# Performance work log

Measured on AMD Instinct MI355X. Metric: run time of the kernel, lower is better.

## Reference

```python
import jax, jax.numpy as jnp
import numpy as np

DN = ('NCHW', 'OIHW', 'NCHW')


def conv(x, W, s, p):
    return jax.lax.conv_general_dilated(x, W, (s, s), [(p, p), (p, p)], dimension_numbers=DN)


def conv_t(y, W, s, p, op):
    # F.conv_transpose2d(y, W, stride=s, padding=p, output_padding=op)
    k = W.shape[2]
    Wt = jnp.flip(W, (2, 3)).transpose(1, 0, 2, 3)  # (I,O,k,k) -> OIHW for the transpose conv
    pad = (k - 1 - p, k - 1 - p + op)
    return jax.lax.conv_general_dilated(y, Wt, (1, 1), [pad, pad], lhs_dilation=(s, s), dimension_numbers=DN)


def build_blk(weight_specs, ms, g, n):
    # blk_diag[r, c, g, m, n'] accumulation exactly as in the torch nested loops
    blk = jnp.zeros((ms, ms, g, n, n), dtype=weight_specs[0][0].dtype)
    for (W, stride, k) in weight_specs:
        A = W.reshape(W.shape[0], g, n, k, k)  # (O, g, n, k, k)
        ATA = jnp.einsum('ogmab,ognab->abgmn', A, A)  # (k, k, g, n, n)
        offset = ((stride - k) // 2) % stride  # k odd branch of the torch code
        for i1 in range(k):
            for j1 in range(k):
                for r in range((i1 + offset) % stride, ms, stride):
                    for c in range((j1 + offset) % stride, ms, stride):
                        blk = blk.at[r, c].add(ATA[i1, j1])
    return blk


def sub_diag(Z, X, blk, ms, g, n):
    b, c, h, w = X.shape
    X0 = X.reshape(b, g, n, h // ms, ms, w // ms, ms)
    Yd = jnp.einsum('rcgmn,bgnhrwc->bgmhrwc', blk, X0)
    return Z - Yd.reshape(b, c, h, w)


def hollow_forward(x0, x1, W00, W10, W11, b0, b1, g):
    # multiply: Y_i = sum_j conv(X_j)
    Y0 = conv(x0, W00, 1, 2)                       # (B,16,258,258)
    Y1 = conv(x0, W10, 2, 3) + conv(x1, W11, 1, 2)  # (B,32,130,130)
    # multiply_transpose: Z_j = sum_i conv_t(Y_i)
    Z0 = conv_t(Y0, W00, 1, 2, 0) + conv_t(Y1, W10, 2, 3, 1)  # (B,16,256,256)
    Z1 = conv_t(Y1, W11, 1, 2, 0)                             # (B,32,128,128)
    # block-diagonal self-term subtraction
    blk0 = build_blk([(W00, 1, 3), (W10, 2, 3)], ms=2, g=1, n=16)
    blk1 = build_blk([(W11, 1, 3)], ms=1, g=2, n=16)
    Z0 = sub_diag(Z0, x0, blk0, 2, 1, 16)
    Z1 = sub_diag(Z1, x1, blk1, 1, 2, 16)
    # bias term: y -= bias/||bias|| * g[i]; return -y
    Z0 = Z0 - (b0 / jnp.linalg.norm(b0)) * g[0]
    Z1 = Z1 - (b1 / jnp.linalg.norm(b1)) * g[1]
    return (-Z0, -Z1)


def setup_inputs() -> dict:
    key = jax.random.key(0)
    ks = jax.random.split(key, 8)
    B = 16
    x0 = jax.random.normal(ks[0], (B, 16, 256, 256), dtype=jnp.float32)
    x1 = jax.random.normal(ks[1], (B, 32, 128, 128), dtype=jnp.float32)
    # conv weights (PyTorch OIHW layout), modest scale ~ 1/sqrt(fan_in*k*k)
    W00 = jax.random.normal(ks[2], (16, 16, 3, 3), dtype=jnp.float32) * 0.08
    W10 = jax.random.normal(ks[3], (32, 16, 3, 3), dtype=jnp.float32) * 0.08
    W11 = jax.random.normal(ks[4], (32, 32, 3, 3), dtype=jnp.float32) * 0.06
    b0 = jax.random.uniform(ks[5], (16, 256, 256), dtype=jnp.float32)
    b1 = jax.random.uniform(ks[6], (32, 128, 128), dtype=jnp.float32)
    g = jnp.ones((2,), dtype=jnp.float32)
    return {'x0': x0, 'x1': x1, 'W00': W00, 'W10': W10, 'W11': W11, 'b0': b0, 'b1': b1, 'g': g}


def reference(x0, x1, W00, W10, W11, b0, b1, g):
    return hollow_forward(x0, x1, W00, W10, W11, b0, b1, g)
```

## Files before the change

### kernel.cpp

```cpp
#include <hip/hip_runtime.h>
#include <stdint.h>


using short8 = __attribute__((ext_vector_type(8))) short;
using f32x4  = __attribute__((ext_vector_type(4))) float;

#define B_ 16

static constexpr size_t Y1T_OFF  = 0;
static constexpr size_t Y1T_ROWB = 132 * 64;
static constexpr size_t X1T_OFF  = (size_t)16 * 130 * 132 * 64;
static constexpr size_t AB0_OFF  = X1T_OFF + (size_t)16 * 128 * 128 * 64;
static constexpr size_t AB1_OFF  = AB0_OFF + 24 * 1024;
static constexpr size_t SUM_OFF  = AB1_OFF + 20 * 1024;
static constexpr size_t AB2_OFF  = SUM_OFF + 1024;
static constexpr size_t PART_OFF = AB2_OFF + 56 * 1024;

__device__ __forceinline__ uint32_t bf16rne(float v) {
  uint32_t u = __float_as_uint(v);
  return (u + 0x7fffu + ((u >> 16) & 1u)) >> 16;
}
__device__ __forceinline__ uint32_t packbf(float lo, float hi) {
  return bf16rne(lo) | (bf16rne(hi) << 16);
}
__device__ __forceinline__ f32x4 mfma16(short8 a, short8 b, f32x4 c) {
  return __builtin_amdgcn_mfma_f32_16x16x32_bf16(a, b, c, 0, 0, 0);
}
__device__ __forceinline__ int xcd_swz(int bid, int chunk) {
  return (bid & 7) * chunk + (bid >> 3);
}

__global__ __launch_bounds__(256) void prep_k(const float* __restrict__ x1,
                                              const float* __restrict__ W00,
                                              const float* __restrict__ W10,
                                              const float* __restrict__ W11,
                                              const float* __restrict__ b0,
                                              const float* __restrict__ b1,
                                              char* __restrict__ ws) {
  __shared__ __align__(16) uint16_t tmp[128 * 32];
  int raw = blockIdx.x, tid = threadIdx.x;

  if (raw < 2048) {
    int b = raw >> 7, r = raw & 127;
    for (int e = tid; e < 4096; e += 256) {
      int ch = e >> 7, c = e & 127;
      float v = x1[((size_t)(b * 32 + ch) * 128 + r) * 128 + c];
      tmp[c * 32 + ch] = (uint16_t)bf16rne(v);
    }
    __syncthreads();
    char* dst = ws + X1T_OFF + ((size_t)(b * 128 + r) * 128) * 64;
    for (int e = tid; e < 512; e += 256)
      *(short8*)(dst + e * 16) = *(const short8*)((const char*)tmp + e * 16);
    return;
  }

  if (raw < 2248) {
    int e = (raw - 2048) * 256 + tid;
    if (e < 12288) {
      int chunk = e >> 9, le = e & 511, lane = le >> 3, j = le & 7;
      int q = lane >> 4, m = lane & 15;
      float val = 0.f;
      if (chunk < 13) {
        int t = 2 * chunk + (q >> 1);
        int n = ((q & 1) << 3) + j;
        if (t <= 24 && t != 12) {
          int dy = t / 5 - 2, dx = t % 5 - 2;
          for (int o = 0; o < 16; ++o) {
            const float* wm = W00 + (o * 16 + m) * 9;
            const float* wn = W00 + (o * 16 + n) * 9;
            for (int ay = 0; ay < 3; ++ay) {
              int ay2 = ay + dy; if ((unsigned)ay2 > 2u) continue;
              for (int ax = 0; ax < 3; ++ax) {
                int ax2 = ax + dx; if ((unsigned)ax2 > 2u) continue;
                val += wm[ay * 3 + ax] * wn[ay2 * 3 + ax2];
              }
            }
          }
        }
      } else if (chunk < 22) {
        int tap = chunk - 13;
        int o = ((lane >> 4) << 3) + j;
        val = W10[(o * 16 + m) * 9 + tap];
      } else {
        int py = chunk - 22;
        int k = ((lane >> 4) << 3) + j;
        int par = k >> 4, n = k & 15;
        for (int o = 0; o < 32; ++o) {
          const float* wn = W10 + (o * 16 + n) * 9;
          const float* wm = W10 + (o * 16 + m) * 9;
          for (int by = 0; by < 3; ++by) {
            if ((py == 0) ? (by != 1) : (by == 1)) continue;
            for (int bx = 0; bx < 3; ++bx) {
              if ((par == 0) ? (bx != 1) : (bx == 1)) continue;
              val -= wn[by * 3 + bx] * wm[by * 3 + bx];
            }
          }
        }
      }
      ((uint16_t*)(ws + AB0_OFF))[chunk * 512 + lane * 8 + j] = (uint16_t)bf16rne(val);
    } else if (e < 12288 + 10240) {
      int e2 = e - 12288;
      int chunk = e2 >> 10, r = e2 & 1023, h = r >> 9, le = r & 511;
      int lane = le >> 3, j = le & 7;
      int m = h * 16 + (lane & 15);
      int kk = ((lane >> 4) << 3) + j;
      float val = 0.f;
      if (chunk < 9) {
        val = W11[(kk * 32 + m) * 9 + chunk];
      } else if ((kk >> 4) == h) {
        int np = kk & 15;
        float s = 0.f;
        for (int o = 0; o < 32; ++o)
          for (int t = 0; t < 9; ++t)
            s += W11[(o * 32 + m) * 9 + t] * W11[(o * 32 + h * 16 + np) * 9 + t];
        val = -s;
      }
      ((uint16_t*)(ws + AB1_OFF))[(chunk * 2 + h) * 512 + lane * 8 + j] = (uint16_t)bf16rne(val);
    } else if (e < 12288 + 10240 + 28672) {
      int e3 = e - 22528;
      int chunk = e3 >> 9, le = e3 & 511;
      int lane = le >> 3, j = le & 7;
      int q = lane >> 4, m = lane & 15;
      int k = q * 8 + j;
      int part;
      float val = 0.f;
      if (chunk < 36) {
        int t = chunk >> 2, h = (chunk >> 1) & 1;
        part = chunk & 1;
        int o = h * 16 + m;
        val = W11[(o * 32 + k) * 9 + t];
      } else {
        int c2 = chunk - 36;
        int c5 = c2 >> 2, h = (c2 >> 1) & 1;
        part = c2 & 1;
        int tap = 2 * c5 + (k >> 4);
        int o = h * 16 + m;
        if (tap <= 8) val = W10[(o * 16 + (k & 15)) * 9 + tap];
      }
      uint32_t hi = bf16rne(val);
      uint16_t outv;
      if (part == 0) outv = (uint16_t)hi;
      else outv = (uint16_t)bf16rne(val - __uint_as_float(hi << 16));
      ((uint16_t*)(ws + AB2_OFF))[chunk * 512 + lane * 8 + j] = outv;
    }
    return;
  }

  float* part = (float*)(ws + PART_OFF);
  if (raw < 2312) {
    int blk = raw - 2248;
    float s = 0.f;
    for (int i = blk * 256 + tid; i < 1048576; i += 64 * 256) {
      float v = b0[i]; s += v * v;
    }
    #pragma unroll
    for (int off = 32; off > 0; off >>= 1) s += __shfl_down(s, off, 64);
    if ((tid & 63) == 0) part[blk * 4 + (tid >> 6)] = s;
  } else {
    int blk = raw - 2312;
    float s = 0.f;
    for (int i = blk * 256 + tid; i < 524288; i += 32 * 256) {
      float v = b1[i]; s += v * v;
    }
    #pragma unroll
    for (int off = 32; off > 0; off >>= 1) s += __shfl_down(s, off, 64);
    if ((tid & 63) == 0) part[256 + blk * 4 + (tid >> 6)] = s;
  }
}

__global__ __launch_bounds__(256, 5) void y1m_k(const float* __restrict__ x0,
                                                char* __restrict__ ws) {
  __shared__ __align__(16) uint16_t x0s[2 * 3 * 2 * 146 * 8];
  int tid = threadIdx.x;
  if (blockIdx.x >= 2080) {
    if (blockIdx.x == 2080) {
      int lane = tid & 63, wvv = tid >> 6;
      const float* part = (const float*)(ws + PART_OFF);
      if (wvv == 0) {
        float s = part[lane * 4] + part[lane * 4 + 1] + part[lane * 4 + 2] + part[lane * 4 + 3];
        #pragma unroll
        for (int off = 32; off > 0; off >>= 1) s += __shfl_down(s, off, 64);
        if (lane == 0) ((float*)(ws + SUM_OFF))[0] = s;
      } else if (wvv == 1) {
        float s = part[256 + lane * 2] + part[256 + lane * 2 + 1];
        #pragma unroll
        for (int off = 32; off > 0; off >>= 1) s += __shfl_down(s, off, 64);
        if (lane == 0) ((float*)(ws + SUM_OFF))[1] = s;
      }
    }
    return;
  }
  int bid = xcd_swz(blockIdx.x, 260);
  int b = bid / 130, iy = bid % 130;

  {
    uint4 z = make_uint4(0u, 0u, 0u, 0u);
    for (int e = tid; e < 1752; e += 256) ((uint4*)x0s)[e] = z;
  }
  __syncthreads();

  {
    const float* x0b = x0 + (size_t)b * 1048576;
    for (int e = tid; e < 6144; e += 256) {
      int r = e >> 11;
      int ch0 = ((e >> 8) & 7) * 2;
      int c = e & 255;
      int gy = 2 * iy + r - 3;
      float v0 = 0.f, v1 = 0.f;
      if ((unsigned)gy < 256u) {
        const float* rp = x0b + (size_t)ch0 * 65536 + (size_t)gy * 256 + c;
        v0 = rp[0]; v1 = rp[65536];
      }
      int sc = c + 3, p = sc & 1, hc = sc >> 1;
      *(uint32_t*)((char*)x0s + ((((ch0 >> 3) * 3 + r) * 2 + p) * 146 + hc) * 16 + (ch0 & 7) * 2)
          = packbf(v0, v1);
    }
  }

  int lane = tid & 63, wv = tid >> 6;
  int nn = lane & 15, q = lane >> 4, qh = q >> 1, ql = q & 1;
  const char* ab2 = ws + AB2_OFF;
  const char* x1tb = ws + X1T_OFF;

  f32x4 a00 = {0.f,0.f,0.f,0.f}, a01 = {0.f,0.f,0.f,0.f};
  f32x4 a10 = {0.f,0.f,0.f,0.f}, a11 = {0.f,0.f,0.f,0.f};
  f32x4 a20 = {0.f,0.f,0.f,0.f}, a21 = {0.f,0.f,0.f,0.f};
  const short8 z8 = {0,0,0,0,0,0,0,0};

  #pragma unroll
  for (int t = 0; t < 9; ++t) {
    const int ay = t / 3, ax = t % 3;
    const char* cb = ab2 + t * 4096 + lane * 16;
    short8 Ah0 = *(const short8*)(cb);
    short8 Al0 = *(const short8*)(cb + 1024);
    short8 Ah1 = *(const short8*)(cb + 2048);
    short8 Al1 = *(const short8*)(cb + 3072);
    int gy = iy + ay - 2;
    bool rowok = ((unsigned)gy < 128u);
    const char* rb = x1tb + ((size_t)(b * 128 + (rowok ? gy : 0))) * 8192 + q * 16;
    int c0 = (wv << 4) + nn + ax - 2;
    bool ok0 = rowok && ((unsigned)c0 < 128u);
    short8 B0 = *(const short8*)(rb + (size_t)(ok0 ? c0 : 0) * 64);
    if (!ok0) B0 = z8;
    int c1 = c0 + 64;
    bool ok1 = rowok && ((unsigned)c1 < 128u);
    short8 B1 = *(const short8*)(rb + (size_t)(ok1 ? c1 : 0) * 64);
    if (!ok1) B1 = z8;
    a00 = mfma16(Ah0, B0, a00); a00 = mfma16(Al0, B0, a00);
    a01 = mfma16(Ah1, B0, a01); a01 = mfma16(Al1, B0, a01);
    a10 = mfma16(Ah0, B1, a10); a10 = mfma16(Al0, B1, a10);
    a11 = mfma16(Ah1, B1, a11); a11 = mfma16(Al1, B1, a11);
    if (wv == 0) {
      int c2 = c0 + 128;
      bool ok2 = rowok && ((unsigned)c2 < 128u);
      short8 B2 = *(const short8*)(rb + (size_t)(ok2 ? c2 : 0) * 64);
      if (!ok2) B2 = z8;
      a20 = mfma16(Ah0, B2, a20); a20 = mfma16(Al0, B2, a20);
      a21 = mfma16(Ah1, B2, a21); a21 = mfma16(Al1, B2, a21);
    }
  }

  __syncthreads();

  #pragma unroll
  for (int c5 = 0; c5 < 5; ++c5) {
    const char* cb = ab2 + (36 + c5 * 4) * 1024 + lane * 16;
    short8 Ah0 = *(const short8*)(cb);
    short8 Al0 = *(const short8*)(cb + 1024);
    short8 Ah1 = *(const short8*)(cb + 2048);
    short8 Al1 = *(const short8*)(cb + 3072);
    int tl = 2 * c5 + qh; if (tl > 8) tl = 8;
    int by = tl / 3, bx = tl % 3;
    int p = bx & 1, hb = bx >> 1;
    const char* bb = (const char*)x0s + ((((ql * 3 + by) * 2 + p) * 146) + hb + nn) * 16 + wv * 256;
    short8 B0 = *(const short8*)(bb);
    short8 B1 = *(const short8*)(bb + 1024);
    a00 = mfma16(Ah0, B0, a00); a00 = mfma16(Al0, B0, a00);
    a01 = mfma16(Ah1, B0, a01); a01 = mfma16(Al1, B0, a01);
    a10 = mfma16(Ah0, B1, a10); a10 = mfma16(Al0, B1, a10);
    a11 = mfma16(Ah1, B1, a11); a11 = mfma16(Al1, B1, a11);
    if (wv == 0) {
      short8 B2 = *(const short8*)(bb + 2048);
      a20 = mfma16(Ah0, B2, a20); a20 = mfma16(Al0, B2, a20);
      a21 = mfma16(Ah1, B2, a21); a21 = mfma16(Al1, B2, a21);
    }
  }

  char* yp = ws + Y1T_OFF + (size_t)(b * 130 + iy) * Y1T_ROWB;
  auto st = [&](int f, f32x4 v0, f32x4 v1) {
    int ix = f * 16 + nn;
    if (ix < 130) {
      uint64_t lo = (uint64_t)packbf(v0[0], v0[1]) | ((uint64_t)packbf(v0[2], v0[3]) << 32);
      uint64_t hi = (uint64_t)packbf(v1[0], v1[1]) | ((uint64_t)packbf(v1[2], v1[3]) << 32);
      *(uint64_t*)(yp + ix * 64 + q * 8) = lo;
      *(uint64_t*)(yp + ix * 64 + 32 + q * 8) = hi;
    }
  };
  st(wv, a00, a01);
  st(wv + 4, a10, a11);
  if (wv == 0) st(8, a20, a21);
}

__global__ __launch_bounds__(256, 5) void outs_k(const float* __restrict__ x0,
                                                 const float* __restrict__ b0,
                                                 const float* __restrict__ b1,
                                                 const float* __restrict__ gg,
                                                 const char* __restrict__ ws,
                                                 float* __restrict__ out) {
  __shared__ __align__(16) uint16_t smem[2 * 5 * 132 * 8 + 4 * 2 * 66 * 8];
  int raw = blockIdx.x, tid = threadIdx.x;
  int lane = tid & 63, wv = tid >> 6;
  int nn = lane & 15, q = lane >> 4;

  if (raw < 8192) {
    uint16_t* x0s = smem;
    uint16_t* y1s = smem + 2 * 5 * 132 * 8;
    int bid = xcd_swz(raw, 1024);
    int b = bid >> 9, jy = (bid >> 1) & 255;
    int jx_base = (bid & 1) << 7;

    {
      const float* x0b = x0 + (size_t)b * 1048576;
      for (int e = tid; e < 1320; e += 256) {
        int c = e % 132, rr = e / 132, r = rr % 5, oct = rr / 5;
        int gy = jy + r - 2, gx = jx_base + c - 2;
        uint32_t w0 = 0u, w1 = 0u, w2 = 0u, w3 = 0u;
        if ((unsigned)gy < 256u && (unsigned)gx < 256u) {
          const float* p = x0b + (size_t)(oct * 8) * 65536 + gy * 256 + gx;
          w0 = packbf(p[0],      p[65536]);
          w1 = packbf(p[131072], p[196608]);
          w2 = packbf(p[262144], p[327680]);
          w3 = packbf(p[393216], p[458752]);
        }
        *(uint4*)((char*)x0s + (size_t)e * 16) = make_uint4(w0, w1, w2, w3);
      }
    }
    {
      const char* y1tb = ws + Y1T_OFF;
      int uy = jy >> 1, c0 = jx_base >> 1;
      for (int e = tid; e < 528; e += 256) {
        int qq = e & 3, t = e >> 2, lc = t % 66, ry = t / 66;
        short8 v = *(const short8*)(y1tb +
            ((size_t)(b * 130 + uy + 1 + ry) * 132 + c0 + lc) * 64 + qq * 16);
        *(short8*)((char*)y1s + ((size_t)(qq * 2 + ry) * 66 + lc) * 16) = v;
      }
    }
    __syncthreads();

    int qh = q >> 1, ql = q & 1;
    const char* ab0 = ws + AB0_OFF;
    f32x4 acc[2];
    #pragma unroll
    for (int i = 0; i < 2; ++i) { acc[i][0]=0.f; acc[i][1]=0.f; acc[i][2]=0.f; acc[i][3]=0.f; }

    const uint16_t* xsl = x0s + ql * 5280;
    const uint16_t* ysl = y1s + q * 1056;
    int pxb = wv * 32 + nn;

    #pragma unroll
    for (int c = 0; c < 13; ++c) {
      short8 A = *(const short8*)(ab0 + c * 1024 + lane * 16);
      const int tA = 2 * c;
      const int tB = (2 * c + 1 > 24) ? 24 : 2 * c + 1;
      const int offA = ((tA / 5) * 132 + (tA % 5)) * 8;
      const int offB = ((tB / 5) * 132 + (tB % 5)) * 8;
      int toff = qh ? offB : offA;
      const uint16_t* base = xsl + toff + pxb * 8;
      short8 B0 = *(const short8*)(base);
      short8 B1 = *(const short8*)(base + 128);
      acc[0] = mfma16(A, B0, acc[0]);
      acc[1] = mfma16(A, B1, acc[1]);
    }

    {
      const short8 z8 = {0,0,0,0,0,0,0,0};
      if ((jy & 1) == 0) {
        #pragma unroll
        for (int bx = 0; bx < 3; ++bx) {
          short8 A = *(const short8*)(ab0 + (16 + bx) * 1024 + lane * 16);
          bool keep = (((nn + 3 - bx) & 1) == 0);
          int cb = (nn + 3 - bx) >> 1;
          const uint16_t* base = ysl + (cb + wv * 16) * 8;
          short8 B0 = *(const short8*)(base);
          short8 B1 = *(const short8*)(base + 64);
          if (!keep) { B0 = z8; B1 = z8; }
          acc[0] = mfma16(A, B0, acc[0]);
          acc[1] = mfma16(A, B1, acc[1]);
        }
      } else {
        #pragma unroll
        for (int s = 0; s < 2; ++s) {
          const int chunkb = s ? 19 : 13;
          const int rybase = s ? 0 : 1;
          #pragma unroll
          for (int bx = 0; bx < 3; ++bx) {
            short8 A = *(const short8*)(ab0 + (chunkb + bx) * 1024 + lane * 16);
            bool keep = (((nn + 3 - bx) & 1) == 0);
            int cb = (nn + 3 - bx) >> 1;
            const uint16_t* base = ysl + (rybase * 66 + cb + wv * 16) * 8;
            short8 B0 = *(const short8*)(base);
            short8 B1 = *(const short8*)(base + 64);
            if (!keep) { B0 = z8; B1 = z8; }
            acc[0] = mfma16(A, B0, acc[0]);
            acc[1] = mfma16(A, B1, acc[1]);
          }
        }
      }
    }

    {
      const short8 z8 = {0,0,0,0,0,0,0,0};
      short8 A = *(const short8*)(ab0 + (22 + (jy & 1)) * 1024 + lane * 16);
      const uint16_t* base = xsl + (2 * 132 + 2) * 8 + pxb * 8;
      short8 B0 = *(const short8*)(base);
      short8 B1 = *(const short8*)(base + 128);
      bool keep = ((nn & 1) == qh);
      if (!keep) { B0 = z8; B1 = z8; }
      acc[0] = mfma16(A, B0, acc[0]);
      acc[1] = mfma16(A, B1, acc[1]);
    }

    float rs0 = gg[0] / sqrtf(((const float*)(ws + SUM_OFF))[0]);
    #pragma unroll
    for (int i = 0; i < 2; ++i) {
      int px = jx_base + wv * 32 + i * 16 + nn;
      #pragma unroll
      for (int reg = 0; reg < 4; ++reg) {
        int m = q * 4 + reg;
        size_t boff = ((size_t)m * 256 + jy) * 256 + px;
        out[((size_t)(b * 16 + m) * 256 + jy) * 256 + px] = b0[boff] * rs0 - acc[i][reg];
      }
    }
    return;
  }

  {
    int bid = xcd_swz(raw - 8192, 256);
    int b = bid >> 7, jy = bid & 127;
    const char* ab1 = ws + AB1_OFF;
    const char* yb = ws + Y1T_OFF + ((size_t)(b * 130 + jy) * 132) * 64 + q * 16;
    const char* xb = ws + X1T_OFF + ((size_t)(b * 128 + jy) * 128) * 64 + q * 16;
    f32x4 acc[2][2];
    #pragma unroll
    for (int i = 0; i < 2; ++i)
      #pragma unroll
      for (int h = 0; h < 2; ++h) { acc[i][h][0]=0.f; acc[i][h][1]=0.f; acc[i][h][2]=0.f; acc[i][h][3]=0.f; }

    int pxb = wv * 32 + nn;

    #pragma unroll
    for (int t = 0; t < 9; ++t) {
      const int ay = t / 3, ax = t % 3;
      short8 A0 = *(const short8*)(ab1 + (t * 2 + 0) * 1024 + lane * 16);
      short8 A1 = *(const short8*)(ab1 + (t * 2 + 1) * 1024 + lane * 16);
      const char* base = yb + (size_t)((2 - ay) * 132 + (2 - ax) + pxb) * 64;
      short8 B0 = *(const short8*)(base);
      short8 B1 = *(const short8*)(base + 1024);
      acc[0][0] = mfma16(A0, B0, acc[0][0]);
      acc[0][1] = mfma16(A1, B0, acc[0][1]);
      acc[1][0] = mfma16(A0, B1, acc[1][0]);
      acc[1][1] = mfma16(A1, B1, acc[1][1]);
    }
    {
      short8 A0 = *(const short8*)(ab1 + 18 * 1024 + lane * 16);
      short8 A1 = *(const short8*)(ab1 + 19 * 1024 + lane * 16);
      const char* base = xb + (size_t)pxb * 64;
      short8 B0 = *(const short8*)(base);
      short8 B1 = *(const short8*)(base + 1024);
      acc[0][0] = mfma16(A0, B0, acc[0][0]);
      acc[0][1] = mfma16(A1, B0, acc[0][1]);
      acc[1][0] = mfma16(A0, B1, acc[1][0]);
      acc[1][1] = mfma16(A1, B1, acc[1][1]);
    }

    float rs1 = gg[1] / sqrtf(((const float*)(ws + SUM_OFF))[1]);
    #pragma unroll
    for (int i = 0; i < 2; ++i) {
      int px = wv * 32 + i * 16 + nn;
      #pragma unroll
      for (int h = 0; h < 2; ++h)
        #pragma unroll
        for (int reg = 0; reg < 4; ++reg) {
          int m = h * 16 + q * 4 + reg;
          size_t boff = ((size_t)m * 128 + jy) * 128 + px;
          out[16777216 + ((size_t)(b * 32 + m) * 128 + jy) * 128 + px] = b1[boff] * rs1 - acc[i][h][reg];
        }
    }
  }
}

extern "C" void kernel_launch(void* const* d_in, const int* in_sizes, int n_in,
                              void* d_out, int out_size, void* d_ws, size_t ws_size,
                              hipStream_t stream) {
  const float* x0  = (const float*)d_in[0];
  const float* x1  = (const float*)d_in[1];
  const float* W00 = (const float*)d_in[2];
  const float* W10 = (const float*)d_in[3];
  const float* W11 = (const float*)d_in[4];
  const float* b0  = (const float*)d_in[5];
  const float* b1  = (const float*)d_in[6];
  const float* g   = (const float*)d_in[7];
  float* out = (float*)d_out;
  char* ws   = (char*)d_ws;

  prep_k<<<2344, 256, 0, stream>>>(x1, W00, W10, W11, b0, b1, ws);
  y1m_k<<<2088, 256, 0, stream>>>(x0, ws);
  outs_k<<<10240, 256, 0, stream>>>(x0, b0, b1, g, ws, out);
}
```

Measured before the change: 319.8 us.

## Prefetch x0 tile into registers and defer LDS stores past first MFMA phase

Zero-filling the whole x0 LDS tile is replaced by zeroing only the padding columns, which drops a barrier. The x0 rows are now read as float2 pairs into 12 register slots before the Y1 MFMA loop and written to LDS only after that loop, so global load latency overlaps with matrix work. This costs 24 extra VGPRs per thread, which may reduce occupancy, and changes the LDS write pattern.

```diff
diff --git a/kernel.cpp b/kernel.cpp
--- a/kernel.cpp
+++ b/kernel.cpp
@@ -195,25 +195,29 @@
 
   {
     uint4 z = make_uint4(0u, 0u, 0u, 0u);
-    for (int e = tid; e < 1752; e += 256) ((uint4*)x0s)[e] = z;
-  }
-  __syncthreads();
-
+    for (int zi = tid; zi < 216; zi += 256) {
+      int pl = zi / 18, k = zi % 18;
+      int hc = (pl & 1) ? (k == 0 ? 0 : k + 128) : (k < 2 ? k : k + 128);
+      *(uint4*)((char*)x0s + (size_t)(pl * 146 + hc) * 16) = z;
+    }
+  }
+
+  uint32_t wlo[12], whi[12];
   {
     const float* x0b = x0 + (size_t)b * 1048576;
-    for (int e = tid; e < 6144; e += 256) {
-      int r = e >> 11;
-      int ch0 = ((e >> 8) & 7) * 2;
-      int c = e & 255;
+    #pragma unroll
+    for (int it = 0; it < 12; ++it) {
+      int e = tid + it * 256;
+      int r = e >> 10, cp = (e >> 3) & 127, ch0 = (e & 7) * 2;
       int gy = 2 * iy + r - 3;
-      float v0 = 0.f, v1 = 0.f;
+      float2 f0 = make_float2(0.f, 0.f), f1 = make_float2(0.f, 0.f);
       if ((unsigned)gy < 256u) {
-        const float* rp = x0b + (size_t)ch0 * 65536 + (size_t)gy * 256 + c;
-        v0 = rp[0]; v1 = rp[65536];
-      }
-      int sc = c + 3, p = sc & 1, hc = sc >> 1;
-      *(uint32_t*)((char*)x0s + ((((ch0 >> 3) * 3 + r) * 2 + p) * 146 + hc) * 16 + (ch0 & 7) * 2)
-          = packbf(v0, v1);
+        const float* rp = x0b + (size_t)ch0 * 65536 + (size_t)gy * 256 + 2 * cp;
+        f0 = *(const float2*)rp;
+        f1 = *(const float2*)(rp + 65536);
+      }
+      wlo[it] = packbf(f0.x, f1.x);
+      whi[it] = packbf(f0.y, f1.y);
     }
   }
 
@@ -260,6 +264,14 @@
     }
   }
 
+  #pragma unroll
+  for (int it = 0; it < 12; ++it) {
+    int e = tid + it * 256;
+    int r = e >> 10, cp = (e >> 3) & 127, ch0 = (e & 7) * 2;
+    char* pbase = (char*)x0s + (size_t)(((ch0 >> 3) * 3 + r) * 2) * 2336 + (ch0 & 7) * 2;
+    *(uint32_t*)(pbase + (size_t)(146 + cp + 1) * 16) = wlo[it];
+    *(uint32_t*)(pbase + (size_t)(cp + 2) * 16)       = whi[it];
+  }
   __syncthreads();
 
   #pragma unroll
```

New measurement: 340.1 us. 6.3% more time.
